# Kernel optimization log

Measured on AMD Instinct MI355X. Metric: run time of the kernel, lower is better.

The kernel has to match this reference:

```python
import jax, jax.numpy as jnp
import numpy as np

K = 16  # neighbors
LEAKY_SLOPE = 0.1  # CamLiFlow uses LeakyReLU(0.1)


def knn_indices(input_xyz, query_xyz, k):
    # input_xyz: [B,3,M], query_xyz: [B,3,N] -> [B,N,k] indices into M
    q = jnp.swapaxes(query_xyz, 1, 2)  # [B,N,3]
    p = jnp.swapaxes(input_xyz, 1, 2)  # [B,M,3]
    d2 = (jnp.sum(q * q, axis=-1)[:, :, None]
          + jnp.sum(p * p, axis=-1)[:, None, :]
          - 2.0 * jnp.einsum('bnc,bmc->bnm', q, p))  # [B,N,M]
    _, idx = jax.lax.top_k(-d2, k)
    return idx


def batch_indexing(x, idx):
    # x: [B,C,M], idx: [B,N,K] -> [B,C,N,K]
    return jax.vmap(lambda xb, ib: xb[:, ib])(x, idx)


def mlp2d(x, layers, act):
    # x: [B,C,N,K]; layers: list of (W[out,in], b[out]); 1x1 conv + act each layer
    for W, b in layers:
        x = act(jnp.einsum('oc,bcnk->bonk', W, x) + b[None, :, None, None])
    return x


def setup_inputs() -> dict:
    key = jax.random.key(0)
    B, N, CIN, COUT = 4, 8192, 64, 64
    ks = jax.random.split(key, 20)
    r = lambda k_, shp: jax.random.normal(k_, shp, dtype=jnp.float32) * 0.1
    return {
        'xyz1': jax.random.normal(ks[0], (B, 3, N), dtype=jnp.float32),
        'feat1': jax.random.normal(ks[1], (B, CIN, N), dtype=jnp.float32),
        'xyz2': jax.random.normal(ks[2], (B, 3, N), dtype=jnp.float32),
        'feat2': jax.random.normal(ks[3], (B, CIN, N), dtype=jnp.float32),
        'cost_w1': r(ks[4], (COUT, 3 + 2 * CIN)),
        'cost_b1': r(ks[5], (COUT,)),
        'cost_w2': r(ks[6], (COUT, COUT)),
        'cost_b2': r(ks[7], (COUT,)),
        'wn1_w1': r(ks[8], (8, 3)), 'wn1_b1': r(ks[9], (8,)),
        'wn1_w2': r(ks[10], (8, 8)), 'wn1_b2': r(ks[11], (8,)),
        'wn1_w3': r(ks[12], (COUT, 8)), 'wn1_b3': r(ks[13], (COUT,)),
        'wn2_w1': r(ks[14], (8, 3)), 'wn2_b1': r(ks[15], (8,)),
        'wn2_w2': r(ks[16], (8, 8)), 'wn2_b2': r(ks[17], (8,)),
        'wn2_w3': r(ks[18], (COUT, 8)), 'wn2_b3': r(ks[19], (COUT,)),
    }


def reference(xyz1, feat1, xyz2, feat2,
              cost_w1, cost_b1, cost_w2, cost_b2,
              wn1_w1, wn1_b1, wn1_w2, wn1_b2, wn1_w3, wn1_b3,
              wn2_w1, wn2_b1, wn2_w2, wn2_b2, wn2_w3, wn2_b3):
    B, Cin, N = feat1.shape
    leaky = lambda v: jax.nn.leaky_relu(v, LEAKY_SLOPE)
    relu = jax.nn.relu

    # Stage 1: point-to-point cost in cloud 2
    idx12 = knn_indices(xyz2, xyz1, K)                       # [B,N,K]
    knn_xyz2 = batch_indexing(xyz2, idx12)                   # [B,3,N,K]
    knn_xyz2_norm = knn_xyz2 - xyz1[:, :, :, None]           # [B,3,N,K]
    knn_feat2 = batch_indexing(feat2, idx12)                 # [B,Cin,N,K]
    feat1_exp = jnp.broadcast_to(feat1[:, :, :, None], (B, Cin, N, K))
    cat = jnp.concatenate([feat1_exp, knn_feat2, knn_xyz2_norm], axis=1)  # [B,2Cin+3,N,K]
    p2p_cost = mlp2d(cat, [(cost_w1, cost_b1), (cost_w2, cost_b2)], leaky)  # [B,Cout,N,K]
    weights2 = mlp2d(knn_xyz2_norm, [(wn2_w1, wn2_b1), (wn2_w2, wn2_b2), (wn2_w3, wn2_b3)], relu)
    p2n_cost = jnp.sum(weights2 * p2p_cost, axis=3)          # [B,Cout,N]

    # Stage 2: aggregate over neighbors in cloud 1
    idx11 = knn_indices(xyz1, xyz1, K)                       # [B,N,K]
    knn_xyz1 = batch_indexing(xyz1, idx11)
    knn_xyz1_norm = knn_xyz1 - xyz1[:, :, :, None]
    weights1 = mlp2d(knn_xyz1_norm, [(wn1_w1, wn1_b1), (wn1_w2, wn1_b2), (wn1_w3, wn1_b3)], relu)
    n2n_cost = batch_indexing(p2n_cost, idx11)               # [B,Cout,N,K]
    n2n_cost = jnp.sum(weights1 * n2n_cost, axis=3)          # [B,Cout,N]
    return n2n_cost  # feat_aligner is Identity (align_channels=None)
```

## Files before the change

kernel.cpp:

```cpp
#include <hip/hip_runtime.h>
#include <stdint.h>

#define BB 4
#define NN 8192
#define KK 16
#define BN (BB*NN)
#define BNK (BN*KK)

__global__ void k_xyzw(const float* __restrict__ xyz1, const float* __restrict__ xyz2,
                       float4* __restrict__ w1, float4* __restrict__ w2){
    int t = blockIdx.x*256 + threadIdx.x;
    if (t >= 2*BN) return;
    const float* src; float4* dst; int i;
    if (t < BN){ src = xyz1; dst = w1; i = t; }
    else       { src = xyz2; dst = w2; i = t - BN; }
    int b = i >> 13, m = i & (NN-1);
    const float* p = src + (size_t)b*3*NN + m;
    float x = p[0], y = p[NN], z = p[2*NN];
    dst[i] = make_float4(x, y, z, x*x + y*y + z*z);
}

__global__ __launch_bounds__(64) void k_prefeat(const float* __restrict__ feat,
                                                const float* __restrict__ W1,
                                                const float* __restrict__ bias, int colOff,
                                                float* __restrict__ out){
    __shared__ float Wt[64*64];
    __shared__ float bsh[64];
    int t = threadIdx.x;
    for (int ci = 0; ci < 64; ++ci)
        Wt[ci*64 + t] = W1[t*131 + colOff + ci];
    bsh[t] = bias ? bias[t] : 0.0f;
    __syncthreads();

    int col = blockIdx.x*64 + t;
    int b = col >> 13, n = col & (NN-1);
    const float* f = feat + (size_t)b*64*NN + n;
    float acc[64];
    #pragma unroll
    for (int co = 0; co < 64; ++co) acc[co] = 0.f;
    for (int ci = 0; ci < 64; ++ci){
        float v = f[(size_t)ci*NN];
        const float4* wrow = (const float4*)(Wt + ci*64);
        #pragma unroll
        for (int c4 = 0; c4 < 16; ++c4){
            float4 w = wrow[c4];
            acc[c4*4+0] = fmaf(w.x, v, acc[c4*4+0]);
            acc[c4*4+1] = fmaf(w.y, v, acc[c4*4+1]);
            acc[c4*4+2] = fmaf(w.z, v, acc[c4*4+2]);
            acc[c4*4+3] = fmaf(w.w, v, acc[c4*4+3]);
        }
    }
    float4* o = (float4*)(out + (size_t)col*64);
    const float4* bs = (const float4*)bsh;
    #pragma unroll
    for (int c4 = 0; c4 < 16; ++c4){
        float4 bb = bs[c4];
        o[c4] = make_float4(acc[c4*4+0]+bb.x, acc[c4*4+1]+bb.y,
                            acc[c4*4+2]+bb.z, acc[c4*4+3]+bb.w);
    }
}

#define SCAP 24
#define CHUNK 1024

__device__ __forceinline__ unsigned long long mono_f64(double d){
    unsigned long long u = (unsigned long long)__double_as_longlong(d);
    return ((long long)u >= 0) ? (u | 0x8000000000000000ull) : ~u;
}

__global__ __launch_bounds__(512) void k_knn(const float4* __restrict__ qpts,
                                             const float4* __restrict__ cA, const float4* __restrict__ cB,
                                             int* __restrict__ outA, int* __restrict__ outB){
    __shared__ unsigned long long mrg[8][64][17];
    const float4* cpts = (blockIdx.y == 0) ? cA : cB;
    int* out            = (blockIdx.y == 0) ? outA : outB;

    int tid = threadIdx.x;
    int lane = tid & 63;
    int wv = tid >> 6;
    int gq = blockIdx.x*64 + lane;
    int b = gq >> 13;
    float4 q = qpts[gq];
    float n2x = -2.f*q.x, n2y = -2.f*q.y, n2z = -2.f*q.z;
    double qx = q.x, qy = q.y, qz = q.z;
    double qq = fma(qx,qx, fma(qy,qy, qz*qz));

    double bd_d[16];
    int bd_i[16];
    #pragma unroll
    for (int i = 0; i < 16; ++i){ bd_d[i] = __builtin_inf(); bd_i[i] = 0x7FFFFFFF; }
    float bdt = __builtin_inff();
    int cnt = 0;
    int* stk = ((int*)mrg) + tid*SCAP;

    const float4* cb = cpts + (size_t)b*NN;

    auto flush = [&](){
        for (int s = 0; s < cnt; ++s){
            int j = stk[s];
            float4 c = cb[j];
            double px = c.x, py = c.y, pz = c.z;
            double pp  = fma(px,px, fma(py,py, pz*pz));
            double dot = fma(qx,px, fma(qy,py, qz*pz));
            double d2 = qq + pp - 2.0*dot;
            if (d2 < bd_d[15]){
                bd_d[15] = d2; bd_i[15] = j;
                #pragma unroll
                for (int jj = 15; jj > 0; --jj){
                    if (bd_d[jj] < bd_d[jj-1]){
                        double td = bd_d[jj]; bd_d[jj] = bd_d[jj-1]; bd_d[jj-1] = td;
                        int    ti = bd_i[jj]; bd_i[jj] = bd_i[jj-1]; bd_i[jj-1] = ti;
                    } else break;
                }
            }
        }
        cnt = 0;
        bdt = (float)(bd_d[15] - qq) + 1e-4f;
    };

    int j0beg = wv*CHUNK;
    for (int j0 = j0beg; j0 < j0beg + CHUNK; j0 += 8){
        #pragma unroll
        for (int jj = 0; jj < 8; ++jj){
            float4 c = cb[j0 + jj];
            float t = fmaf(n2x, c.x, c.w);
            t = fmaf(n2y, c.y, t);
            t = fmaf(n2z, c.z, t);
            if (t < bdt){ stk[cnt] = j0 + jj; cnt++; }
        }
        if (__any(cnt >= 16)) flush();
    }
    flush();

    __syncthreads();
    #pragma unroll
    for (int i = 0; i < 16; ++i){
        unsigned long long key = mono_f64(bd_d[i]);
        mrg[wv][lane][i] = (key & ~8191ull) | (unsigned long long)(unsigned)bd_i[i];
    }
    __syncthreads();

    if (tid < 64){
        unsigned long long hv[8];
        int hp[8];
        #pragma unroll
        for (int c = 0; c < 8; ++c){ hv[c] = mrg[c][tid][0]; hp[c] = 1; }
        int* o = out + (size_t)(blockIdx.x*64 + tid)*16;
        for (int i = 0; i < 16; ++i){
            unsigned long long best = ~0ull; int bc = 0;
            #pragma unroll
            for (int c = 0; c < 8; ++c){
                if (hv[c] < best){ best = hv[c]; bc = c; }
            }
            o[i] = (int)(best & 8191ull);
            #pragma unroll
            for (int c = 0; c < 8; ++c){
                if (c == bc){
                    hv[c] = (hp[c] < 16) ? mrg[c][tid][hp[c]] : ~0ull;
                    hp[c]++;
                }
            }
        }
    }
}

__global__ __launch_bounds__(256) void k_h2(const float4* __restrict__ qpts, const float4* __restrict__ cpts,
                                            const int* __restrict__ idx,
                                            const float* __restrict__ w1, const float* __restrict__ b1,
                                            const float* __restrict__ w2, const float* __restrict__ b2,
                                            float* __restrict__ H){
    int i = blockIdx.x*256 + threadIdx.x;
    int gq = i >> 4;
    int b = gq >> 13;
    int m = idx[i];
    float4 p = cpts[b*NN + m];
    float4 q = qpts[gq];
    float x = p.x - q.x, y = p.y - q.y, z = p.z - q.z;
    float h1[8], h2[8];
    #pragma unroll
    for (int j = 0; j < 8; ++j){
        float v = b1[j] + w1[j*3+0]*x + w1[j*3+1]*y + w1[j*3+2]*z;
        h1[j] = fmaxf(v, 0.f);
    }
    #pragma unroll
    for (int j = 0; j < 8; ++j){
        float v = b2[j];
        #pragma unroll
        for (int jj = 0; jj < 8; ++jj) v = fmaf(w2[j*8+jj], h1[jj], v);
        h2[j] = fmaxf(v, 0.f);
    }
    float4* o = (float4*)(H + (size_t)i*8);
    o[0] = make_float4(h2[0],h2[1],h2[2],h2[3]);
    o[1] = make_float4(h2[4],h2[5],h2[6],h2[7]);
}

__device__ __forceinline__ float rl_f(int hb, int lane_c){
    return __int_as_float(__builtin_amdgcn_readlane(hb, lane_c));
}

__global__ __launch_bounds__(256) void k_stage1(const float* __restrict__ A1, const float* __restrict__ A2,
                                                const int* __restrict__ idx12, const float* __restrict__ H12,
                                                const float4* __restrict__ xyzw1, const float4* __restrict__ xyzw2,
                                                const float* __restrict__ W1full, const float* __restrict__ W2,
                                                const float* __restrict__ b2, const float* __restrict__ w3,
                                                const float* __restrict__ b3, float* __restrict__ p2n){
    int lane = threadIdx.x & 63;
    int wv = threadIdx.x >> 6;
    int wgid = blockIdx.x*4 + wv;

    float w2r[64];
    const float4* w2p = (const float4*)(W2 + (size_t)lane*64);
    #pragma unroll
    for (int c4 = 0; c4 < 16; ++c4){
        float4 v = w2p[c4];
        w2r[c4*4+0]=v.x; w2r[c4*4+1]=v.y; w2r[c4*4+2]=v.z; w2r[c4*4+3]=v.w;
    }
    float w1cx = W1full[lane*131+128], w1cy = W1full[lane*131+129], w1cz = W1full[lane*131+130];
    float b2v = b2[lane], b3v = b3[lane];
    float w3r[8];
    {
        const float4* w3p = (const float4*)(w3 + (size_t)lane*8);
        float4 a = w3p[0], bq = w3p[1];
        w3r[0]=a.x; w3r[1]=a.y; w3r[2]=a.z; w3r[3]=a.w;
        w3r[4]=bq.x; w3r[5]=bq.y; w3r[6]=bq.z; w3r[7]=bq.w;
    }

    for (int task = wgid; task < BN; task += 4096){
        int b = task >> 13;
        float4 q = xyzw1[task];
        float a1 = A1[(size_t)task*64 + lane];
        float acc = 0.f;
        const int* ip = idx12 + (size_t)task*16;
        for (int k = 0; k < 16; ++k){
            int m = ip[k];
            float4 p = xyzw2[b*NN + m];
            float a2 = A2[(size_t)(b*NN+m)*64 + lane];
            float h = a1 + a2;
            h = fmaf(w1cx, p.x - q.x, h);
            h = fmaf(w1cy, p.y - q.y, h);
            h = fmaf(w1cz, p.z - q.z, h);
            h = fmaxf(h, 0.1f*h);
            int hb = __float_as_int(h);
            float c20 = 0.f, c21 = 0.f, c22 = 0.f, c23 = 0.f;
            #pragma unroll
            for (int c = 0; c < 64; c += 4){
                c20 = fmaf(w2r[c+0], rl_f(hb, c+0), c20);
                c21 = fmaf(w2r[c+1], rl_f(hb, c+1), c21);
                c22 = fmaf(w2r[c+2], rl_f(hb, c+2), c22);
                c23 = fmaf(w2r[c+3], rl_f(hb, c+3), c23);
            }
            float c2 = ((c20 + c21) + (c22 + c23)) + b2v;
            c2 = fmaxf(c2, 0.1f*c2);
            const float4* hw = (const float4*)(H12 + (size_t)(task*16+k)*8);
            float4 ha = hw[0], hb2 = hw[1];
            float w = b3v;
            w = fmaf(w3r[0], ha.x, w); w = fmaf(w3r[1], ha.y, w);
            w = fmaf(w3r[2], ha.z, w); w = fmaf(w3r[3], ha.w, w);
            w = fmaf(w3r[4], hb2.x, w); w = fmaf(w3r[5], hb2.y, w);
            w = fmaf(w3r[6], hb2.z, w); w = fmaf(w3r[7], hb2.w, w);
            w = fmaxf(w, 0.f);
            acc = fmaf(w, c2, acc);
        }
        p2n[(size_t)task*64 + lane] = acc;
    }
}

__global__ __launch_bounds__(256) void k_stage2(const float* __restrict__ p2n, const int* __restrict__ idx11,
                                                const float* __restrict__ H11, const float* __restrict__ w3,
                                                const float* __restrict__ b3, float* __restrict__ out){
    __shared__ float tl[64*65];
    int lane = threadIdx.x & 63;
    int wv = threadIdx.x >> 6;
    int base = blockIdx.x*64;
    int b = base >> 13;

    float w3r[8];
    {
        const float4* w3p = (const float4*)(w3 + (size_t)lane*8);
        float4 a = w3p[0], bq = w3p[1];
        w3r[0]=a.x; w3r[1]=a.y; w3r[2]=a.z; w3r[3]=a.w;
        w3r[4]=bq.x; w3r[5]=bq.y; w3r[6]=bq.z; w3r[7]=bq.w;
    }
    float b3v = b3[lane];

    for (int i = 0; i < 16; ++i){
        int col = base + wv*16 + i;
        const int* ip = idx11 + (size_t)col*16;
        const float* Hb = H11 + (size_t)col*16*8;
        float acc = 0.f;
        for (int k = 0; k < 16; ++k){
            int m = ip[k];
            float c = p2n[(size_t)(b*NN + m)*64 + lane];
            const float4* hw = (const float4*)(Hb + k*8);
            float4 ha = hw[0], hb2 = hw[1];
            float w = b3v;
            w = fmaf(w3r[0], ha.x, w);  w = fmaf(w3r[1], ha.y, w);
            w = fmaf(w3r[2], ha.z, w);  w = fmaf(w3r[3], ha.w, w);
            w = fmaf(w3r[4], hb2.x, w); w = fmaf(w3r[5], hb2.y, w);
            w = fmaf(w3r[6], hb2.z, w); w = fmaf(w3r[7], hb2.w, w);
            w = fmaxf(w, 0.f);
            acc = fmaf(w, c, acc);
        }
        tl[(wv*16+i)*65 + lane] = acc;
    }
    __syncthreads();
    int n0 = base & (NN-1);
    #pragma unroll
    for (int i = 0; i < 16; ++i){
        int co = i*4 + wv;
        float v = tl[lane*65 + co];
        out[((size_t)b*64 + co)*NN + n0 + lane] = v;
    }
}

extern "C" void kernel_launch(void* const* d_in, const int* in_sizes, int n_in,
                              void* d_out, int out_size, void* d_ws, size_t ws_size,
                              hipStream_t stream) {
    const float* xyz1   = (const float*)d_in[0];
    const float* feat1  = (const float*)d_in[1];
    const float* xyz2   = (const float*)d_in[2];
    const float* feat2  = (const float*)d_in[3];
    const float* cost_w1 = (const float*)d_in[4];
    const float* cost_b1 = (const float*)d_in[5];
    const float* cost_w2 = (const float*)d_in[6];
    const float* cost_b2 = (const float*)d_in[7];
    const float* wn1_w1 = (const float*)d_in[8];
    const float* wn1_b1 = (const float*)d_in[9];
    const float* wn1_w2 = (const float*)d_in[10];
    const float* wn1_b2 = (const float*)d_in[11];
    const float* wn1_w3 = (const float*)d_in[12];
    const float* wn1_b3 = (const float*)d_in[13];
    const float* wn2_w1 = (const float*)d_in[14];
    const float* wn2_b1 = (const float*)d_in[15];
    const float* wn2_w2 = (const float*)d_in[16];
    const float* wn2_b2 = (const float*)d_in[17];
    const float* wn2_w3 = (const float*)d_in[18];
    const float* wn2_b3 = (const float*)d_in[19];

    char* ws = (char*)d_ws;
    float4* xyzw1 = (float4*)(ws + 0);
    float4* xyzw2 = (float4*)(ws + 524288);
    float*  A1    = (float*)(ws + 1048576);
    float*  A2    = (float*)(ws + 9437184);
    int*    idx12 = (int*)  (ws + 17825792);
    int*    idx11 = (int*)  (ws + 19922944);
    float*  H12   = (float*)(ws + 22020096);
    float*  H11   = (float*)(ws + 38797312);
    float*  p2n   = (float*)(ws + 55574528);

    k_xyzw<<<256, 256, 0, stream>>>(xyz1, xyz2, xyzw1, xyzw2);
    k_prefeat<<<512, 64, 0, stream>>>(feat1, cost_w1, cost_b1, 0,  A1);
    k_prefeat<<<512, 64, 0, stream>>>(feat2, cost_w1, nullptr, 64, A2);
    k_knn<<<dim3(512,2), 512, 0, stream>>>(xyzw1, xyzw2, xyzw1, idx12, idx11);
    k_h2<<<2048, 256, 0, stream>>>(xyzw1, xyzw2, idx12, wn2_w1, wn2_b1, wn2_w2, wn2_b2, H12);
    k_h2<<<2048, 256, 0, stream>>>(xyzw1, xyzw1, idx11, wn1_w1, wn1_b1, wn1_w2, wn1_b2, H11);
    k_stage1<<<1024, 256, 0, stream>>>(A1, A2, idx12, H12, xyzw1, xyzw2,
                                       cost_w1, cost_w2, cost_b2, wn2_w3, wn2_b3, p2n);
    k_stage2<<<512, 256, 0, stream>>>(p2n, idx11, H11, wn1_w3, wn1_b3, (float*)d_out);
}
```

Baseline: 820.1 us.

## Share KNN pruning threshold across waves and use branchless packed-key insertion

Each query is handled by 8 waves that scan separate candidate chunks. The waves now share a per-query distance threshold in shared memory through atomicMin, so each wave can prune candidates using the best bound found by any wave. The top-16 list becomes packed 64-bit keys (distance bits plus index) kept sorted with a branchless compare-swap network. The final serial 8-way merge is replaced by a tree reduction with early exit, the output is written as int4, and the stack size and unroll are reduced. The risks are atomic traffic on every flush, extra barriers in the merge tree, and low-order distance bits lost in the packed keys affecting tie order.

```diff
diff --git a/kernel.cpp b/kernel.cpp
--- a/kernel.cpp
+++ b/kernel.cpp
@@ -60,18 +60,32 @@
     }
 }
 
-#define SCAP 24
+#define SCAP 19
 #define CHUNK 1024
 
+__device__ __forceinline__ unsigned mono_f32(float f){
+    unsigned u = __float_as_uint(f);
+    return ((int)u >= 0) ? (u | 0x80000000u) : ~u;
+}
+__device__ __forceinline__ float unmono_f32(unsigned v){
+    unsigned u = ((int)v < 0) ? (v & 0x7FFFFFFFu) : ~v;
+    return __uint_as_float(u);
+}
 __device__ __forceinline__ unsigned long long mono_f64(double d){
     unsigned long long u = (unsigned long long)__double_as_longlong(d);
     return ((long long)u >= 0) ? (u | 0x8000000000000000ull) : ~u;
 }
+__device__ __forceinline__ double unmono_f64(unsigned long long v){
+    unsigned long long u = ((long long)v < 0) ? (v & 0x7FFFFFFFFFFFFFFFull) : ~v;
+    return __longlong_as_double((long long)u);
+}
 
 __global__ __launch_bounds__(512) void k_knn(const float4* __restrict__ qpts,
                                              const float4* __restrict__ cA, const float4* __restrict__ cB,
                                              int* __restrict__ outA, int* __restrict__ outB){
-    __shared__ unsigned long long mrg[8][64][17];
+    __shared__ unsigned int thrsh[64];
+    __shared__ __align__(16) char pool[38912];
+
     const float4* cpts = (blockIdx.y == 0) ? cA : cB;
     int* out            = (blockIdx.y == 0) ? outA : outB;
 
@@ -85,14 +99,16 @@
     double qx = q.x, qy = q.y, qz = q.z;
     double qq = fma(qx,qx, fma(qy,qy, qz*qz));
 
-    double bd_d[16];
-    int bd_i[16];
-    #pragma unroll
-    for (int i = 0; i < 16; ++i){ bd_d[i] = __builtin_inf(); bd_i[i] = 0x7FFFFFFF; }
+    if (tid < 64) thrsh[tid] = 0xFF800000u;
+    __syncthreads();
+
+    unsigned long long A[16];
+    #pragma unroll
+    for (int i = 0; i < 16; ++i) A[i] = 0xFFF0000000000000ull | 8191ull;
+
     float bdt = __builtin_inff();
     int cnt = 0;
-    int* stk = ((int*)mrg) + tid*SCAP;
-
+    int* stk = ((int*)pool) + tid*SCAP;
     const float4* cb = cpts + (size_t)b*NN;
 
     auto flush = [&](){
@@ -103,64 +119,81 @@
             double pp  = fma(px,px, fma(py,py, pz*pz));
             double dot = fma(qx,px, fma(qy,py, qz*pz));
             double d2 = qq + pp - 2.0*dot;
-            if (d2 < bd_d[15]){
-                bd_d[15] = d2; bd_i[15] = j;
+            unsigned long long key = (mono_f64(d2) & ~8191ull) | (unsigned long long)(unsigned)j;
+            if (key < A[15]){
+                A[15] = key;
                 #pragma unroll
-                for (int jj = 15; jj > 0; --jj){
-                    if (bd_d[jj] < bd_d[jj-1]){
-                        double td = bd_d[jj]; bd_d[jj] = bd_d[jj-1]; bd_d[jj-1] = td;
-                        int    ti = bd_i[jj]; bd_i[jj] = bd_i[jj-1]; bd_i[jj-1] = ti;
-                    } else break;
+                for (int jj = 15; jj >= 1; --jj){
+                    unsigned long long lo = A[jj-1], hi = A[jj];
+                    bool sw = hi < lo;
+                    A[jj]   = sw ? lo : hi;
+                    A[jj-1] = sw ? hi : lo;
                 }
             }
         }
         cnt = 0;
-        bdt = (float)(bd_d[15] - qq) + 1e-4f;
+        float scr = (float)(unmono_f64(A[15]) - qq);
+        unsigned m = mono_f32(scr);
+        unsigned old = atomicMin(&thrsh[lane], m);
+        bdt = unmono_f32(old < m ? old : m) + 1e-4f;
     };
 
     int j0beg = wv*CHUNK;
-    for (int j0 = j0beg; j0 < j0beg + CHUNK; j0 += 8){
-        #pragma unroll
-        for (int jj = 0; jj < 8; ++jj){
-            float4 c = cb[j0 + jj];
-            float t = fmaf(n2x, c.x, c.w);
-            t = fmaf(n2y, c.y, t);
-            t = fmaf(n2z, c.z, t);
-            if (t < bdt){ stk[cnt] = j0 + jj; cnt++; }
-        }
-        if (__any(cnt >= 16)) flush();
+    for (int jo = j0beg; jo < j0beg + CHUNK; jo += 128){
+        {
+            float f = unmono_f32(thrsh[lane]) + 1e-4f;
+            bdt = fminf(bdt, f);
+        }
+        for (int j0 = jo; j0 < jo + 128; j0 += 4){
+            const float4* cp = cb + j0;
+            #pragma unroll
+            for (int jj = 0; jj < 4; ++jj){
+                float4 c = cp[jj];
+                float t = fmaf(n2x, c.x, c.w);
+                t = fmaf(n2y, c.y, t);
+                t = fmaf(n2z, c.z, t);
+                if (t < bdt){ stk[cnt] = j0 + jj; cnt++; }
+            }
+            if (__any(cnt >= 16)) flush();
+        }
     }
     flush();
 
     __syncthreads();
-    #pragma unroll
-    for (int i = 0; i < 16; ++i){
-        unsigned long long key = mono_f64(bd_d[i]);
-        mrg[wv][lane][i] = (key & ~8191ull) | (unsigned long long)(unsigned)bd_i[i];
-    }
-    __syncthreads();
-
-    if (tid < 64){
-        unsigned long long hv[8];
-        int hp[8];
-        #pragma unroll
-        for (int c = 0; c < 8; ++c){ hv[c] = mrg[c][tid][0]; hp[c] = 1; }
-        int* o = out + (size_t)(blockIdx.x*64 + tid)*16;
-        for (int i = 0; i < 16; ++i){
-            unsigned long long best = ~0ull; int bc = 0;
+    unsigned long long* mrg = (unsigned long long*)pool;
+    #pragma unroll
+    for (int r = 4; r >= 1; r >>= 1){
+        if (wv >= r && wv < 2*r){
+            unsigned long long* dst = mrg + ((size_t)(wv - r)*64 + lane)*17;
             #pragma unroll
-            for (int c = 0; c < 8; ++c){
-                if (hv[c] < best){ best = hv[c]; bc = c; }
-            }
-            o[i] = (int)(best & 8191ull);
-            #pragma unroll
-            for (int c = 0; c < 8; ++c){
-                if (c == bc){
-                    hv[c] = (hp[c] < 16) ? mrg[c][tid][hp[c]] : ~0ull;
-                    hp[c]++;
+            for (int i = 0; i < 16; ++i) dst[i] = A[i];
+        }
+        __syncthreads();
+        if (wv < r){
+            const unsigned long long* src = mrg + ((size_t)wv*64 + lane)*17;
+            for (int i = 0; i < 16; ++i){
+                unsigned long long bkey = src[i];
+                if (__all(bkey >= A[15])) break;
+                if (bkey < A[15]){
+                    A[15] = bkey;
+                    #pragma unroll
+                    for (int jj = 15; jj >= 1; --jj){
+                        unsigned long long lo = A[jj-1], hi = A[jj];
+                        bool sw = hi < lo;
+                        A[jj]   = sw ? lo : hi;
+                        A[jj-1] = sw ? hi : lo;
+                    }
                 }
             }
         }
+        __syncthreads();
+    }
+    if (wv == 0){
+        int4* o = (int4*)(out + (size_t)gq*16);
+        #pragma unroll
+        for (int i = 0; i < 4; ++i)
+            o[i] = make_int4((int)(A[i*4+0] & 8191ull), (int)(A[i*4+1] & 8191ull),
+                             (int)(A[i*4+2] & 8191ull), (int)(A[i*4+3] & 8191ull));
     }
 }
 
```

Result: faster. 742.3 us (-9.5%).
